# Kernel tuning notes

Hardware: AMD Instinct MI355X
Metric: run time of the kernel (lower is better)

## Reference

```python
import jax, jax.numpy as jnp
import numpy as np

IN_F = 16      # in_features
OUT_F = 64     # out_features
LAT = 128      # latent_dimension
HID = 1024     # hidden_dim
NH = 3         # n_harmonics
NE = 2         # n_eig
K = NH * NE    # 6, fourier coeff width (must be 6: n_range hardcoded to [0,1,2])
M = (IN_F + 1) * OUT_F            # per-sample weight+bias size
CS = (M + 2) * K                  # coeffs_size = 6540
BATCH = 8192


def setup_inputs() -> dict:
    key = jax.random.key(0)
    ks = jax.random.split(key, 7)
    sc = lambda n: np.float32(1.0 / np.sqrt(n))
    x = jax.random.normal(ks[0], (BATCH, IN_F + LAT + 1), jnp.float32)
    W1 = jax.random.normal(ks[1], (LAT, HID), jnp.float32) * sc(LAT)
    b1 = jax.random.normal(ks[2], (HID,), jnp.float32) * sc(LAT)
    W2 = jax.random.normal(ks[3], (HID, CS), jnp.float32) * sc(HID)
    b2 = jax.random.normal(ks[4], (CS,), jnp.float32) * sc(HID)
    W3 = jax.random.normal(ks[5], (CS, CS), jnp.float32) * sc(CS)
    b3 = jax.random.normal(ks[6], (CS,), jnp.float32) * sc(CS)
    return {"x": x, "W1": W1, "b1": b1, "W2": W2, "b2": b2, "W3": W3, "b3": b3}


def reference(x, W1, b1, W2, b2, W3, b3):
    B = x.shape[0]
    s = x[-1, IN_F]                 # scalar time, as in torch code
    inp = x[:, :IN_F]               # [B, in]
    z = x[:, -LAT:]                 # [B, latent]
    # CoeffDecoder: tanh(fc1) -> tanh(fc2) -> fc3
    h = jnp.tanh(z @ W1 + b1)
    h = jnp.tanh(h @ W2 + b2)
    coeffs = h @ W3 + b3            # [B, CS]
    coeff = coeffs[:, : M * K].reshape(B, M, K)          # [B, M, 6]
    dilation = coeffs[:, M * K : (M + 1) * K]            # [B, 6]
    shift = coeffs[:, (M + 1) * K :]                     # [B, 6]
    sv = s * dilation + shift                            # [B, 6]
    n_range = jnp.arange(3, dtype=x.dtype)               # hardcoded [0,1,2]
    # diag_embed(cos)+diag_embed(sin) then bmm(...).sum(2) collapses to a
    # per-sample dot with the diagonal values (row-sums of the diag matrices)
    v = jnp.concatenate(
        [jnp.cos(sv[:, :3] * n_range), jnp.sin(sv[:, 3:] * n_range)], axis=1
    )                                                    # [B, 6]
    w = jnp.einsum("bmk,bk->bm", coeff, v)               # [B, M]
    weight = w[:, : IN_F * OUT_F].reshape(B, IN_F, OUT_F)
    bias = w[:, IN_F * OUT_F : M]                        # [B, out]
    return jnp.einsum("bi,bio->bo", inp, weight) + bias  # [B, out]
```

## Files before the change

### kernel.cpp

```cpp
#include <hip/hip_runtime.h>
#include <hip/hip_bf16.h>
#include <cmath>

#define B_     8192
#define INF_   16
#define LAT_   128
#define HID_   1024
#define CS_    6540
#define XCOLS_ 145
#define MK_    6528
#define NW_    1088
#define KP_    6656
#define N3_    6528

typedef _Float16 f16;
typedef _Float16 f16x8 __attribute__((ext_vector_type(8)));
typedef float    f32x4 __attribute__((ext_vector_type(4)));

__global__ __launch_bounds__(256) void zh_kernel(const float* __restrict__ x,
                                                 f16* __restrict__ zh) {
  int t = blockIdx.x * 256 + threadIdx.x;
  int b = t >> 7, j = t & 127;
  zh[t] = (f16)x[(size_t)b * XCOLS_ + 17 + j];
}

__global__ __launch_bounds__(256) void tconv_kernel(const float* __restrict__ src,
                                                    f16* __restrict__ dst,
                                                    int Ks, int Ns, int Nlim,
                                                    int Kp, int Np) {
  __shared__ float tile[64][65];
  int k0 = blockIdx.x * 64, n0 = blockIdx.y * 64;
  int tx = threadIdx.x & 63, ty = threadIdx.x >> 6;
#pragma unroll
  for (int i = 0; i < 16; ++i) {
    int r = i * 4 + ty;
    int gk = k0 + r, gn = n0 + tx;
    tile[r][tx] = (gk < Ks && gn < Nlim) ? src[(size_t)gk * Ns + gn] : 0.f;
  }
  __syncthreads();
#pragma unroll
  for (int i = 0; i < 16; ++i) {
    int n = i * 4 + ty;
    int gn = n0 + n, gk = k0 + tx;
    if (gn < Np && gk < Kp) dst[(size_t)gn * Kp + gk] = (f16)tile[tx][n];
  }
}

template <int ROWS>
__device__ __forceinline__ void stage_tile(const f16* __restrict__ src, int ld,
                                           int row0, int k0, f16* lds, int tid) {
  constexpr int ISSUES = ROWS / 32;
  const int l = tid & 63, w = tid >> 6;
#pragma unroll
  for (int i = 0; i < ISSUES; ++i) {
    int chunk = i * 4096 + w * 1024;
    int o = chunk + l * 16;
    int r = o >> 7;
    int p = o ^ ((r & 7) << 4);
    int c = (p & 127) >> 1;
    const f16* g = src + (size_t)(row0 + r) * ld + k0 + c;
    __builtin_amdgcn_global_load_lds(
        (const __attribute__((address_space(1))) void*)g,
        (__attribute__((address_space(3))) void*)(lds + (chunk >> 1)),
        16, 0, 0);
  }
}

__device__ __forceinline__ f16x8 frag_ld(const f16* base, int row, int kb) {
  int off = row * 128 + (kb ^ ((row & 7) << 4));
  return *(const f16x8*)((const char*)base + off);
}

template <int BN, int EPI>
__global__ __launch_bounds__(256) void gemm_nt(
    const f16* __restrict__ A, int lda, const f16* __restrict__ Bt, int ldb,
    const float* __restrict__ bias, int blim, f16* __restrict__ outh, int ldo,
    float* __restrict__ w, const float* __restrict__ vv, int Ksteps, int nbn) {
  constexpr int NI = BN / 32;
  constexpr int WCOL = BN / 2;
  constexpr int STAGE = (128 + BN) * 64 * 2;
  constexpr int EPIB = (EPI == 1) ? 128 * 97 * 4 : 0;
  constexpr int SMEM = STAGE > EPIB ? STAGE : EPIB;
  __shared__ __align__(16) unsigned char smem[SMEM];
  f16* As = (f16*)smem;
  f16* Bs = As + 128 * 64;

  const int tid = threadIdx.x;
  const int l = tid & 63, wid = tid >> 6;
  const int wr = wid >> 1, wc = wid & 1;
  const int l15 = l & 15, lg = l >> 4;
  const int bm = blockIdx.x / nbn, bn = blockIdx.x % nbn;
  const int m0 = bm * 128, n0 = bn * BN;

  f32x4 acc[4][NI];
#pragma unroll
  for (int mi = 0; mi < 4; ++mi)
#pragma unroll
    for (int ni = 0; ni < NI; ++ni) acc[mi][ni] = (f32x4){0.f, 0.f, 0.f, 0.f};

  for (int ks = 0; ks < Ksteps; ++ks) {
    const int k0 = ks * 64;
    stage_tile<128>(A, lda, m0, k0, As, tid);
    stage_tile<BN>(Bt, ldb, n0, k0, Bs, tid);
    __syncthreads();
#pragma unroll
    for (int kk = 0; kk < 64; kk += 32) {
      const int kb = (kk + lg * 8) * 2;
      f16x8 af[4];
#pragma unroll
      for (int mi = 0; mi < 4; ++mi)
        af[mi] = frag_ld(As, wr * 64 + mi * 16 + l15, kb);
#pragma unroll
      for (int ni = 0; ni < NI; ++ni) {
        f16x8 bf = frag_ld(Bs, wc * WCOL + ni * 16 + l15, kb);
#pragma unroll
        for (int mi = 0; mi < 4; ++mi)
          acc[mi][ni] = __builtin_amdgcn_mfma_f32_16x16x32_f16(af[mi], bf,
                                                               acc[mi][ni], 0, 0, 0);
      }
    }
    __syncthreads();
  }

  if constexpr (EPI == 0) {
#pragma unroll
    for (int ni = 0; ni < NI; ++ni) {
      int col = n0 + wc * WCOL + ni * 16 + l15;
      float bv = (col < blim) ? bias[col] : 0.f;
#pragma unroll
      for (int mi = 0; mi < 4; ++mi) {
        int r0 = m0 + wr * 64 + mi * 16 + lg * 4;
#pragma unroll
        for (int j = 0; j < 4; ++j)
          outh[(size_t)(r0 + j) * ldo + col] = (f16)tanhf(acc[mi][ni][j] + bv);
      }
    }
  } else {
    float* Cl = (float*)smem;
#pragma unroll
    for (int ni = 0; ni < NI; ++ni) {
      int cl = wc * WCOL + ni * 16 + l15;
      float bv = bias[n0 + cl];
#pragma unroll
      for (int mi = 0; mi < 4; ++mi) {
        int rl = wr * 64 + mi * 16 + lg * 4;
#pragma unroll
        for (int j = 0; j < 4; ++j) Cl[(rl + j) * 97 + cl] = acc[mi][ni][j] + bv;
      }
    }
    __syncthreads();
#pragma unroll
    for (int it = 0; it < 8; ++it) {
      int idx = it * 256 + tid;
      int r = idx >> 4, g = idx & 15;
      const float* vr = vv + (size_t)(m0 + r) * 8;
      float s = 0.f;
#pragma unroll
      for (int k = 0; k < 6; ++k) s += Cl[r * 97 + g * 6 + k] * vr[k];
      w[(size_t)(m0 + r) * NW_ + bn * 16 + g] = s;
    }
  }
}

__global__ __launch_bounds__(256) void sv_kernel(const f16* __restrict__ h2,
                                                 const float* __restrict__ W3,
                                                 const float* __restrict__ b3,
                                                 const float* __restrict__ x,
                                                 float* __restrict__ vv) {
  __shared__ float red[12][4];
  int b = blockIdx.x, tid = threadIdx.x;
  int lane = tid & 63, wid = tid >> 6;
  float p[12];
#pragma unroll
  for (int j = 0; j < 12; ++j) p[j] = 0.f;
  for (int k = tid; k < CS_; k += 256) {
    float hv = (float)h2[(size_t)b * KP_ + k];
    const float* wr = W3 + (size_t)k * CS_ + MK_;
#pragma unroll
    for (int j = 0; j < 12; ++j) p[j] += hv * wr[j];
  }
#pragma unroll
  for (int j = 0; j < 12; ++j) {
    float v = p[j];
    for (int off = 32; off; off >>= 1) v += __shfl_down(v, off, 64);
    if (lane == 0) red[j][wid] = v;
  }
  __syncthreads();
  if (tid < 6) {
    int j = tid;
    float dil = red[j][0] + red[j][1] + red[j][2] + red[j][3] + b3[MK_ + j];
    float sh  = red[6 + j][0] + red[6 + j][1] + red[6 + j][2] + red[6 + j][3] + b3[MK_ + 6 + j];
    float s = x[(size_t)(B_ - 1) * XCOLS_ + INF_];
    float sv = s * dil + sh;
    vv[(size_t)b * 8 + j] = (j < 3) ? cosf(sv * (float)j) : sinf(sv * (float)(j - 3));
  }
}

__global__ __launch_bounds__(256) void out_kernel(const float* __restrict__ x,
                                                  const float* __restrict__ w,
                                                  float* __restrict__ out) {
  int wid = threadIdx.x >> 6, lane = threadIdx.x & 63;
  int b = blockIdx.x * 4 + wid;
  const float* wr = w + (size_t)b * NW_;
  const float* xr = x + (size_t)b * XCOLS_;
  float acc = wr[1024 + lane];
#pragma unroll
  for (int i = 0; i < 16; ++i) acc += xr[i] * wr[i * 64 + lane];
  out[(size_t)b * 64 + lane] = acc;
}

extern "C" void kernel_launch(void* const* d_in, const int* in_sizes, int n_in,
                              void* d_out, int out_size, void* d_ws, size_t ws_size,
                              hipStream_t stream) {
  const float* x  = (const float*)d_in[0];
  const float* W1 = (const float*)d_in[1];
  const float* b1 = (const float*)d_in[2];
  const float* W2 = (const float*)d_in[3];
  const float* b2 = (const float*)d_in[4];
  const float* W3 = (const float*)d_in[5];
  const float* b3 = (const float*)d_in[6];
  float* out = (float*)d_out;

  char* ws = (char*)d_ws;
  f16*   zh  = (f16*)(ws);
  f16*   W1t = (f16*)(ws + 2097152);
  f16*   W2t = (f16*)(ws + 2359296);
  f16*   W3t = (f16*)(ws + 15990784);
  f16*   h1  = (f16*)(ws + 102891520);
  f16*   h2  = (f16*)(ws + 119668736);
  float* vv  = (float*)(ws + 228720640);
  float* w   = (float*)(ws + 228982784);

  zh_kernel<<<4096, 256, 0, stream>>>(x, zh);
  tconv_kernel<<<dim3(2, 16),    256, 0, stream>>>(W1, W1t, 128,  1024, 1024, 128,  1024);
  tconv_kernel<<<dim3(16, 104),  256, 0, stream>>>(W2, W2t, 1024, CS_,  CS_,  1024, KP_);
  tconv_kernel<<<dim3(104, 102), 256, 0, stream>>>(W3, W3t, CS_,  CS_,  N3_,  KP_,  N3_);

  gemm_nt<128, 0><<<(1024 / 128) * (B_ / 128), 256, 0, stream>>>(
      zh, 128, W1t, 128, b1, 1024, h1, 1024, nullptr, nullptr, 2, 1024 / 128);
  gemm_nt<128, 0><<<(KP_ / 128) * (B_ / 128), 256, 0, stream>>>(
      h1, 1024, W2t, 1024, b2, CS_, h2, KP_, nullptr, nullptr, 16, KP_ / 128);
  sv_kernel<<<B_, 256, 0, stream>>>(h2, W3, b3, x, vv);
  gemm_nt<96, 1><<<(N3_ / 96) * (B_ / 128), 256, 0, stream>>>(
      h2, KP_, W3t, KP_, b3, N3_, nullptr, 0, w, vv, KP_ / 64, N3_ / 96);
  out_kernel<<<B_ / 4, 256, 0, stream>>>(x, w, out);
}
```

Before: 1.722 ms.

## Add double-buffered 256x192 GEMM3 kernel and vectorize sv with transposed dilation weights

Replaces the third GEMM with a dedicated 512-thread kernel using 256x192 tiles and double-buffered LDS staging via global_load_lds. It uses explicit vmcnt waits, barriers and setprio to overlap loads with MFMA work, and an XCD-aware block remap. The sv kernel now reads a small transposed f16 copy of the 12 dilation/shift columns (reusing the zh buffer after GEMM1) with vector loads, replacing strided fp32 reads of W3. The large LDS footprint (112KB) limits occupancy to one block per CU, and the hand-placed waitcnts carry correctness risk.

```diff
diff --git a/kernel.cpp b/kernel.cpp
--- a/kernel.cpp
+++ b/kernel.cpp
@@ -17,6 +17,11 @@
 typedef _Float16 f16x8 __attribute__((ext_vector_type(8)));
 typedef float    f32x4 __attribute__((ext_vector_type(4)));
 
+#define VMCNT(n) do { asm volatile("s_waitcnt vmcnt(" #n ")" ::: "memory"); \
+                      __builtin_amdgcn_sched_barrier(0); } while (0)
+#define LGKMCNT0 do { asm volatile("s_waitcnt lgkmcnt(0)" ::: "memory"); \
+                      __builtin_amdgcn_sched_barrier(0); } while (0)
+
 __global__ __launch_bounds__(256) void zh_kernel(const float* __restrict__ x,
                                                  f16* __restrict__ zh) {
   int t = blockIdx.x * 256 + threadIdx.x;
@@ -44,6 +49,11 @@
     int gn = n0 + n, gk = k0 + tx;
     if (gn < Np && gk < Kp) dst[(size_t)gn * Kp + gk] = (f16)tile[tx][n];
   }
+}
+
+__device__ __forceinline__ f16x8 frag_ld(const f16* base, int row, int kb) {
+  int off = row * 128 + (kb ^ ((row & 7) << 4));
+  return *(const f16x8*)((const char*)base + off);
 }
 
 template <int ROWS>
@@ -66,23 +76,32 @@
   }
 }
 
-__device__ __forceinline__ f16x8 frag_ld(const f16* base, int row, int kb) {
-  int off = row * 128 + (kb ^ ((row & 7) << 4));
-  return *(const f16x8*)((const char*)base + off);
-}
-
-template <int BN, int EPI>
+template <int ROWS>
+__device__ __forceinline__ void stage512(const f16* __restrict__ src,
+                                         int row0, int k0, f16* lds, int tid) {
+  constexpr int ISSUES = ROWS / 64;
+  const int l = tid & 63, w = tid >> 6;
+#pragma unroll
+  for (int i = 0; i < ISSUES; ++i) {
+    int chunk = i * 8192 + w * 1024;
+    int o = chunk + l * 16;
+    int r = o >> 7;
+    int p = o ^ ((r & 7) << 4);
+    int c = (p & 127) >> 1;
+    const f16* g = src + (size_t)(row0 + r) * KP_ + k0 + c;
+    __builtin_amdgcn_global_load_lds(
+        (const __attribute__((address_space(1))) void*)g,
+        (__attribute__((address_space(3))) void*)(lds + (chunk >> 1)),
+        16, 0, 0);
+  }
+}
+
 __global__ __launch_bounds__(256) void gemm_nt(
     const f16* __restrict__ A, int lda, const f16* __restrict__ Bt, int ldb,
     const float* __restrict__ bias, int blim, f16* __restrict__ outh, int ldo,
-    float* __restrict__ w, const float* __restrict__ vv, int Ksteps, int nbn) {
-  constexpr int NI = BN / 32;
-  constexpr int WCOL = BN / 2;
-  constexpr int STAGE = (128 + BN) * 64 * 2;
-  constexpr int EPIB = (EPI == 1) ? 128 * 97 * 4 : 0;
-  constexpr int SMEM = STAGE > EPIB ? STAGE : EPIB;
-  __shared__ __align__(16) unsigned char smem[SMEM];
-  f16* As = (f16*)smem;
+    int Ksteps, int nbn) {
+  __shared__ __align__(16) f16 smem[(128 + 128) * 64];
+  f16* As = smem;
   f16* Bs = As + 128 * 64;
 
   const int tid = threadIdx.x;
@@ -90,18 +109,18 @@
   const int wr = wid >> 1, wc = wid & 1;
   const int l15 = l & 15, lg = l >> 4;
   const int bm = blockIdx.x / nbn, bn = blockIdx.x % nbn;
-  const int m0 = bm * 128, n0 = bn * BN;
-
-  f32x4 acc[4][NI];
+  const int m0 = bm * 128, n0 = bn * 128;
+
+  f32x4 acc[4][4];
 #pragma unroll
   for (int mi = 0; mi < 4; ++mi)
 #pragma unroll
-    for (int ni = 0; ni < NI; ++ni) acc[mi][ni] = (f32x4){0.f, 0.f, 0.f, 0.f};
+    for (int ni = 0; ni < 4; ++ni) acc[mi][ni] = (f32x4){0.f, 0.f, 0.f, 0.f};
 
   for (int ks = 0; ks < Ksteps; ++ks) {
     const int k0 = ks * 64;
     stage_tile<128>(A, lda, m0, k0, As, tid);
-    stage_tile<BN>(Bt, ldb, n0, k0, Bs, tid);
+    stage_tile<128>(Bt, ldb, n0, k0, Bs, tid);
     __syncthreads();
 #pragma unroll
     for (int kk = 0; kk < 64; kk += 32) {
@@ -111,8 +130,8 @@
       for (int mi = 0; mi < 4; ++mi)
         af[mi] = frag_ld(As, wr * 64 + mi * 16 + l15, kb);
 #pragma unroll
-      for (int ni = 0; ni < NI; ++ni) {
-        f16x8 bf = frag_ld(Bs, wc * WCOL + ni * 16 + l15, kb);
+      for (int ni = 0; ni < 4; ++ni) {
+        f16x8 bf = frag_ld(Bs, wc * 64 + ni * 16 + l15, kb);
 #pragma unroll
         for (int mi = 0; mi < 4; ++mi)
           acc[mi][ni] = __builtin_amdgcn_mfma_f32_16x16x32_f16(af[mi], bf,
@@ -122,48 +141,141 @@
     __syncthreads();
   }
 
-  if constexpr (EPI == 0) {
-#pragma unroll
-    for (int ni = 0; ni < NI; ++ni) {
-      int col = n0 + wc * WCOL + ni * 16 + l15;
-      float bv = (col < blim) ? bias[col] : 0.f;
-#pragma unroll
-      for (int mi = 0; mi < 4; ++mi) {
-        int r0 = m0 + wr * 64 + mi * 16 + lg * 4;
-#pragma unroll
-        for (int j = 0; j < 4; ++j)
-          outh[(size_t)(r0 + j) * ldo + col] = (f16)tanhf(acc[mi][ni][j] + bv);
+#pragma unroll
+  for (int ni = 0; ni < 4; ++ni) {
+    int col = n0 + wc * 64 + ni * 16 + l15;
+    float bv = (col < blim) ? bias[col] : 0.f;
+#pragma unroll
+    for (int mi = 0; mi < 4; ++mi) {
+      int r0 = m0 + wr * 64 + mi * 16 + lg * 4;
+#pragma unroll
+      for (int j = 0; j < 4; ++j)
+        outh[(size_t)(r0 + j) * ldo + col] = (f16)tanhf(acc[mi][ni][j] + bv);
+    }
+  }
+}
+
+#define G3_KSTEPS 104
+__global__ __launch_bounds__(512) void gemm3_kernel(
+    const f16* __restrict__ A,
+    const f16* __restrict__ Bt,
+    const float* __restrict__ bias,
+    const float* __restrict__ vv,
+    float* __restrict__ w) {
+  __shared__ __align__(16) unsigned char smem[114688];
+  f16* Asb = (f16*)smem;
+  f16* Bsb = Asb + 2 * 256 * 64;
+
+  const int tid = threadIdx.x;
+  const int l = tid & 63, wid = tid >> 6;
+  const int wr = wid >> 2, wc = wid & 3;
+  const int l15 = l & 15, lg = l >> 4;
+  const int wg = (blockIdx.x & 7) * 136 + (blockIdx.x >> 3);
+  const int bm = wg / 34, bn = wg % 34;
+  const int m0 = bm * 256, n0 = bn * 192;
+
+  f32x4 acc[8][3];
+#pragma unroll
+  for (int mi = 0; mi < 8; ++mi)
+#pragma unroll
+    for (int ni = 0; ni < 3; ++ni) acc[mi][ni] = (f32x4){0.f, 0.f, 0.f, 0.f};
+
+  stage512<256>(A, m0, 0, Asb, tid);
+  stage512<192>(Bt, n0, 0, Bsb, tid);
+  stage512<256>(A, m0, 64, Asb + 256 * 64, tid);
+  stage512<192>(Bt, n0, 64, Bsb + 192 * 64, tid);
+  VMCNT(7);
+  __builtin_amdgcn_s_barrier();
+
+#pragma unroll 1
+  for (int ks = 0; ks < G3_KSTEPS; ++ks) {
+    const f16* Ac = Asb + (ks & 1) * 256 * 64;
+    const f16* Bc = Bsb + (ks & 1) * 192 * 64;
+#pragma unroll
+    for (int kki = 0; kki < 2; ++kki) {
+      const int kb = (kki * 32 + lg * 8) * 2;
+      f16x8 bf[3], af[4];
+#pragma unroll
+      for (int ni = 0; ni < 3; ++ni)
+        bf[ni] = frag_ld(Bc, wc * 48 + ni * 16 + l15, kb);
+#pragma unroll
+      for (int mi = 0; mi < 4; ++mi)
+        af[mi] = frag_ld(Ac, wr * 128 + mi * 16 + l15, kb);
+      __builtin_amdgcn_s_barrier();
+      LGKMCNT0;
+      __builtin_amdgcn_s_setprio(1);
+#pragma unroll
+      for (int mi = 0; mi < 4; ++mi)
+#pragma unroll
+        for (int ni = 0; ni < 3; ++ni)
+          acc[mi][ni] = __builtin_amdgcn_mfma_f32_16x16x32_f16(af[mi], bf[ni],
+                                                               acc[mi][ni], 0, 0, 0);
+      __builtin_amdgcn_s_setprio(0);
+      __builtin_amdgcn_s_barrier();
+#pragma unroll
+      for (int mi = 0; mi < 4; ++mi)
+        af[mi] = frag_ld(Ac, wr * 128 + (mi + 4) * 16 + l15, kb);
+      __builtin_amdgcn_s_barrier();
+      LGKMCNT0;
+      __builtin_amdgcn_s_setprio(1);
+#pragma unroll
+      for (int mi = 0; mi < 4; ++mi)
+#pragma unroll
+        for (int ni = 0; ni < 3; ++ni)
+          acc[mi + 4][ni] = __builtin_amdgcn_mfma_f32_16x16x32_f16(af[mi], bf[ni],
+                                                                   acc[mi + 4][ni], 0, 0, 0);
+      __builtin_amdgcn_s_setprio(0);
+      __builtin_amdgcn_s_barrier();
+    }
+    if (ks + 1 < G3_KSTEPS) {
+      __builtin_amdgcn_sched_barrier(0);
+      if (ks + 2 < G3_KSTEPS) {
+        f16* An = Asb + (ks & 1) * 256 * 64;
+        f16* Bn = Bsb + (ks & 1) * 192 * 64;
+        stage512<256>(A, m0, (ks + 2) * 64, An, tid);
+        stage512<192>(Bt, n0, (ks + 2) * 64, Bn, tid);
+        VMCNT(7);
+      } else {
+        VMCNT(0);
       }
-    }
-  } else {
-    float* Cl = (float*)smem;
-#pragma unroll
-    for (int ni = 0; ni < NI; ++ni) {
-      int cl = wc * WCOL + ni * 16 + l15;
-      float bv = bias[n0 + cl];
-#pragma unroll
-      for (int mi = 0; mi < 4; ++mi) {
-        int rl = wr * 64 + mi * 16 + lg * 4;
-#pragma unroll
-        for (int j = 0; j < 4; ++j) Cl[(rl + j) * 97 + cl] = acc[mi][ni][j] + bv;
+      __builtin_amdgcn_s_barrier();
+    }
+  }
+
+  float* Cl = (float*)smem;
+#pragma unroll
+  for (int h = 0; h < 2; ++h) {
+    __syncthreads();
+    if (wr == h) {
+#pragma unroll
+      for (int ni = 0; ni < 3; ++ni) {
+        int cl = wc * 48 + ni * 16 + l15;
+        float bv = bias[n0 + cl];
+#pragma unroll
+        for (int mi = 0; mi < 8; ++mi) {
+          int rl = mi * 16 + lg * 4;
+#pragma unroll
+          for (int j = 0; j < 4; ++j)
+            Cl[(rl + j) * 193 + cl] = acc[mi][ni][j] + bv;
+        }
       }
     }
     __syncthreads();
 #pragma unroll
     for (int it = 0; it < 8; ++it) {
-      int idx = it * 256 + tid;
-      int r = idx >> 4, g = idx & 15;
-      const float* vr = vv + (size_t)(m0 + r) * 8;
+      int idx = it * 512 + tid;
+      int r = idx >> 5, g = idx & 31;
+      const float* vr = vv + (size_t)(m0 + h * 128 + r) * 8;
       float s = 0.f;
 #pragma unroll
-      for (int k = 0; k < 6; ++k) s += Cl[r * 97 + g * 6 + k] * vr[k];
-      w[(size_t)(m0 + r) * NW_ + bn * 16 + g] = s;
+      for (int k = 0; k < 6; ++k) s += Cl[r * 193 + g * 6 + k] * vr[k];
+      w[(size_t)(m0 + h * 128 + r) * NW_ + bn * 32 + g] = s;
     }
   }
 }
 
 __global__ __launch_bounds__(256) void sv_kernel(const f16* __restrict__ h2,
-                                                 const float* __restrict__ W3,
+                                                 const f16* __restrict__ dil12,
                                                  const float* __restrict__ b3,
                                                  const float* __restrict__ x,
                                                  float* __restrict__ vv) {
@@ -173,11 +285,16 @@
   float p[12];
 #pragma unroll
   for (int j = 0; j < 12; ++j) p[j] = 0.f;
-  for (int k = tid; k < CS_; k += 256) {
-    float hv = (float)h2[(size_t)b * KP_ + k];
-    const float* wr = W3 + (size_t)k * CS_ + MK_;
-#pragma unroll
-    for (int j = 0; j < 12; ++j) p[j] += hv * wr[j];
+  for (int c = tid; c < KP_ / 8; c += 256) {
+    f16x8 hv = *(const f16x8*)(h2 + (size_t)b * KP_ + c * 8);
+#pragma unroll
+    for (int j = 0; j < 12; ++j) {
+      f16x8 wv = *(const f16x8*)(dil12 + (size_t)j * KP_ + c * 8);
+      float s = 0.f;
+#pragma unroll
+      for (int e = 0; e < 8; ++e) s += (float)hv[e] * (float)wv[e];
+      p[j] += s;
+    }
   }
 #pragma unroll
   for (int j = 0; j < 12; ++j) {
@@ -230,18 +347,19 @@
   f16*   h2  = (f16*)(ws + 119668736);
   float* vv  = (float*)(ws + 228720640);
   float* w   = (float*)(ws + 228982784);
+  f16*   dil12 = zh;
 
   zh_kernel<<<4096, 256, 0, stream>>>(x, zh);
   tconv_kernel<<<dim3(2, 16),    256, 0, stream>>>(W1, W1t, 128,  1024, 1024, 128,  1024);
   tconv_kernel<<<dim3(16, 104),  256, 0, stream>>>(W2, W2t, 1024, CS_,  CS_,  1024, KP_);
   tconv_kernel<<<dim3(104, 102), 256, 0, stream>>>(W3, W3t, CS_,  CS_,  N3_,  KP_,  N3_);
 
-  gemm_nt<128, 0><<<(1024 / 128) * (B_ / 128), 256, 0, stream>>>(
-      zh, 128, W1t, 128, b1, 1024, h1, 1024, nullptr, nullptr, 2, 1024 / 128);
-  gemm_nt<128, 0><<<(KP_ / 128) * (B_ / 128), 256, 0, stream>>>(
-      h1, 1024, W2t, 1024, b2, CS_, h2, KP_, nullptr, nullptr, 16, KP_ / 128);
-  sv_kernel<<<B_, 256, 0, stream>>>(h2, W3, b3, x, vv);
-  gemm_nt<96, 1><<<(N3_ / 96) * (B_ / 128), 256, 0, stream>>>(
-      h2, KP_, W3t, KP_, b3, N3_, nullptr, 0, w, vv, KP_ / 64, N3_ / 96);
+  gemm_nt<<<(1024 / 128) * (B_ / 128), 256, 0, stream>>>(
+      zh, 128, W1t, 128, b1, 1024, h1, 1024, 2, 1024 / 128);
+  tconv_kernel<<<dim3(104, 1),   256, 0, stream>>>(W3 + MK_, dil12, CS_, CS_, 12, KP_, 12);
+  gemm_nt<<<(KP_ / 128) * (B_ / 128), 256, 0, stream>>>(
+      h1, 1024, W2t, 1024, b2, CS_, h2, KP_, 16, KP_ / 128);
+  sv_kernel<<<B_, 256, 0, stream>>>(h2, dil12, b3, x, vv);
+  gemm3_kernel<<<(B_ / 256) * (N3_ / 192), 512, 0, stream>>>(h2, W3t, b3, vv, w);
   out_kernel<<<B_ / 4, 256, 0, stream>>>(x, w, out);
 }
```

Result: faster. 1.396 ms (-18.9%).
